# Kernel tuning notes

Measured on AMD Instinct MI355X. Metric: run time of the kernel, lower is better.

## Reference

```python
import jax, jax.numpy as jnp
import numpy as np

N, E, B = 8000, 128000, 16
DIN, D, H, C, L = 16, 256, 8, 32, 6
MC, NT = 200, 8
NEG_SLOPE = 0.2


def layernorm(x, s, b):
    mu = jnp.mean(x, axis=-1, keepdims=True)
    var = jnp.mean(jnp.square(x - mu), axis=-1, keepdims=True)
    return (x - mu) * jax.lax.rsqrt(var + 1e-5) * s + b


def setup_inputs() -> dict:
    key = jax.random.key(0)
    ks = iter(jax.random.split(key, 64))
    rn = lambda shape, s=0.05: jax.random.normal(next(ks), shape, jnp.float32) * s
    inp = {}
    inp['x'] = jax.random.normal(next(ks), (N, DIN), jnp.float32)
    inp['edge_index'] = jax.random.randint(next(ks), (2, E), 0, N)
    inp['batch'] = jnp.sort(jax.random.randint(next(ks), (N,), 0, B))
    # node encoder: Linear(DIN,D) + LayerNorm
    inp['enc_W'] = rn((DIN, D)); inp['enc_b'] = jnp.zeros((D,), jnp.float32)
    inp['enc_ls'] = jnp.ones((D,), jnp.float32); inp['enc_lb'] = jnp.zeros((D,), jnp.float32)
    # GATv2 layers (stacked): lin_l, lin_r, att, output bias, post LayerNorm
    inp['Wl'] = rn((L, D, D)); inp['bl'] = jnp.zeros((L, D), jnp.float32)
    inp['Wr'] = rn((L, D, D)); inp['br'] = jnp.zeros((L, D), jnp.float32)
    inp['att'] = rn((L, H, C))
    inp['gb'] = jnp.zeros((L, D), jnp.float32)
    inp['gls'] = jnp.ones((L, D), jnp.float32); inp['glb'] = jnp.zeros((L, D), jnp.float32)
    # color head MLP: D -> D -> D//2 -> MC
    inp['cW1'] = rn((D, D)); inp['cb1'] = jnp.zeros((D,), jnp.float32)
    inp['cW2'] = rn((D, D // 2)); inp['cb2'] = jnp.zeros((D // 2,), jnp.float32)
    inp['cW3'] = rn((D // 2, MC)); inp['cb3'] = jnp.zeros((MC,), jnp.float32)
    # chromatic head: 2D -> D -> D//2 -> MC
    inp['chW1'] = rn((2 * D, D)); inp['chb1'] = jnp.zeros((D,), jnp.float32)
    inp['chW2'] = rn((D, D // 2)); inp['chb2'] = jnp.zeros((D // 2,), jnp.float32)
    inp['chW3'] = rn((D // 2, MC)); inp['chb3'] = jnp.zeros((MC,), jnp.float32)
    # type head: 2D -> 128 -> NT
    inp['tW1'] = rn((2 * D, 128)); inp['tb1'] = jnp.zeros((128,), jnp.float32)
    inp['tW2'] = rn((128, NT)); inp['tb2'] = jnp.zeros((NT,), jnp.float32)
    # difficulty head: 2D -> 64 -> 1, sigmoid * 100
    inp['dW1'] = rn((2 * D, 64)); inp['db1'] = jnp.zeros((64,), jnp.float32)
    inp['dW2'] = rn((64, 1)); inp['db2'] = jnp.zeros((1,), jnp.float32)
    return inp


def reference(x, edge_index, batch, enc_W, enc_b, enc_ls, enc_lb,
              Wl, bl, Wr, br, att, gb, gls, glb,
              cW1, cb1, cW2, cb2, cW3, cb3,
              chW1, chb1, chW2, chb2, chW3, chb3,
              tW1, tb1, tW2, tb2, dW1, db1, dW2, db2):
    n = x.shape[0]
    # node encoder (dropout = identity at inference)
    h = jax.nn.relu(layernorm(x @ enc_W + enc_b, enc_ls, enc_lb))
    # add self loops once (same for every layer)
    sl = jnp.arange(n)
    src = jnp.concatenate([edge_index[0], sl])  # message source j
    dst = jnp.concatenate([edge_index[1], sl])  # message target i
    for i in range(L):
        xl = (h @ Wl[i] + bl[i]).reshape(n, H, C)  # source transform
        xr = (h @ Wr[i] + br[i]).reshape(n, H, C)  # target transform
        # GATv2 attention: a^T LeakyReLU(xl_j + xr_i)
        e = jax.nn.leaky_relu(xl[src] + xr[dst], NEG_SLOPE)  # [E+N, H, C]
        logits = jnp.einsum('ehc,hc->eh', e, att[i])          # [E+N, H]
        # segment softmax over destination node (self-loops guarantee denom > 0)
        m = jax.ops.segment_max(logits, dst, num_segments=n)
        m = jnp.where(jnp.isfinite(m), m, 0.0)
        p = jnp.exp(logits - m[dst])
        denom = jax.ops.segment_sum(p, dst, num_segments=n)
        alpha = p / denom[dst]
        out = jax.ops.segment_sum(xl[src] * alpha[:, :, None], dst, num_segments=n)
        out = out.reshape(n, D) + gb[i]
        h_new = jax.nn.elu(layernorm(out, gls[i], glb[i]))
        h = h + h_new if i > 0 else h_new
    # per-node color logits
    z = jax.nn.relu(h @ cW1 + cb1)
    z = jax.nn.relu(z @ cW2 + cb2)
    node_colors = z @ cW3 + cb3
    # global mean/max pooling per graph
    cnt = jax.ops.segment_sum(jnp.ones((n,), h.dtype), batch, num_segments=B)
    mean_p = jax.ops.segment_sum(h, batch, num_segments=B) / jnp.maximum(cnt, 1.0)[:, None]
    max_p = jax.ops.segment_max(h, batch, num_segments=B)
    max_p = jnp.where(jnp.isfinite(max_p), max_p, 0.0)
    g = jnp.concatenate([mean_p, max_p], axis=1)  # [B, 2D]
    zc = jax.nn.relu(g @ chW1 + chb1)
    zc = jax.nn.relu(zc @ chW2 + chb2)
    chromatic_num = zc @ chW3 + chb3
    zt = jax.nn.relu(g @ tW1 + tb1)
    graph_type = zt @ tW2 + tb2
    zd = jax.nn.relu(g @ dW1 + db1)
    difficulty = jax.nn.sigmoid(zd @ dW2 + db2) * 100.0
    return (node_colors, chromatic_num, graph_type, difficulty)
```

## Files before the change

### kernel.cpp

```cpp
#include <hip/hip_runtime.h>
#include <hip/hip_bf16.h>

constexpr int DIN = 16;
constexpr int D   = 256;
constexpr int NH  = 8;
constexpr int NC  = 32;
constexpr int MC  = 200;
constexpr int NT  = 8;
constexpr int BG  = 16;
constexpr int NL  = 6;
constexpr int PS  = 16;
constexpr float NEG = 0.2f;

typedef __attribute__((ext_vector_type(8))) short bfrag;
typedef __attribute__((ext_vector_type(4))) float f32x4;

__device__ inline unsigned short f2bf(float f) {
    unsigned int u = __float_as_uint(f);
    u += 0x7FFFu + ((u >> 16) & 1u);
    return (unsigned short)(u >> 16);
}
__device__ inline float bf2f(unsigned short u) {
    return __uint_as_float((unsigned int)u << 16);
}

__device__ inline float dot_ilp(const float* g, const float* __restrict__ W, int K, int ldw, int t) {
    float a0 = 0.f, a1 = 0.f, a2 = 0.f, a3 = 0.f;
    for (int k = 0; k < K; k += 4) {
        a0 = fmaf(g[k + 0], W[(k + 0) * ldw + t], a0);
        a1 = fmaf(g[k + 1], W[(k + 1) * ldw + t], a1);
        a2 = fmaf(g[k + 2], W[(k + 2) * ldw + t], a2);
        a3 = fmaf(g[k + 3], W[(k + 3) * ldw + t], a3);
    }
    return (a0 + a1) + (a2 + a3);
}


__device__ inline void enc_node(const float* x, const float* W, const float* b, const float* ls,
                                const float* lb, float* h, int n, int lane) {
    int c4 = lane * 4;
    float xs[DIN];
#pragma unroll
    for (int k = 0; k < DIN; k += 4) {
        float4 xv = *(const float4*)&x[n * DIN + k];
        xs[k] = xv.x; xs[k + 1] = xv.y; xs[k + 2] = xv.z; xs[k + 3] = xv.w;
    }
    float4 a = *(const float4*)&b[c4];
#pragma unroll
    for (int k = 0; k < DIN; k++) {
        float4 wv = *(const float4*)&W[k * D + c4];
        a.x = fmaf(xs[k], wv.x, a.x);
        a.y = fmaf(xs[k], wv.y, a.y);
        a.z = fmaf(xs[k], wv.z, a.z);
        a.w = fmaf(xs[k], wv.w, a.w);
    }
    float s = a.x + a.y + a.z + a.w;
#pragma unroll
    for (int msk = 1; msk <= 32; msk <<= 1) s += __shfl_xor(s, msk);
    float mu = s * (1.f / D);
    float4 dv = make_float4(a.x - mu, a.y - mu, a.z - mu, a.w - mu);
    float v2 = dv.x * dv.x + dv.y * dv.y + dv.z * dv.z + dv.w * dv.w;
#pragma unroll
    for (int msk = 1; msk <= 32; msk <<= 1) v2 += __shfl_xor(v2, msk);
    float rstd = rsqrtf(v2 * (1.f / D) + 1e-5f);
    float4 lsv = *(const float4*)&ls[c4];
    float4 lbv = *(const float4*)&lb[c4];
    float4 y = make_float4(fmaxf(dv.x * rstd * lsv.x + lbv.x, 0.f),
                           fmaxf(dv.y * rstd * lsv.y + lbv.y, 0.f),
                           fmaxf(dv.z * rstd * lsv.z + lbv.z, 0.f),
                           fmaxf(dv.w * rstd * lsv.w + lbv.w, 0.f));
    *(float4*)&h[(size_t)n * D + c4] = y;
}

__device__ inline float4 attn_compute(const unsigned short* xl, const unsigned short* xr,
                                      const int* row_ptr, const int* col, const float* att,
                                      const float* gb, const float* gls, const float* glb,
                                      const float* h, int layer, int n, int lane) {
    int c4 = lane * 4;
    ushort4 xr4 = *(const ushort4*)&xr[(size_t)n * D + c4];
    float4 xrv = make_float4(bf2f(xr4.x), bf2f(xr4.y), bf2f(xr4.z), bf2f(xr4.w));
    float4 av  = *(const float4*)&att[c4];
    int beg = row_ptr[n], end = row_ptr[n + 1];
    int deg = end - beg;
    int myc = col[beg + min(lane, deg - 1)];
    float l = 0.f;
    float4 acc = make_float4(0.f, 0.f, 0.f, 0.f);
    auto loadx = [&](int i) -> ushort4 {
        if (i < deg) {
            int s = (i < 64) ? __shfl(myc, i) : col[beg + i];
            return *(const ushort4*)&xl[(size_t)s * D + c4];
        }
        return make_ushort4(0, 0, 0, 0);
    };
    auto step = [&](ushort4 x4) {
        float4 xlv = make_float4(bf2f(x4.x), bf2f(x4.y), bf2f(x4.z), bf2f(x4.w));
        float sx = xlv.x + xrv.x; sx = sx > 0.f ? sx : NEG * sx;
        float sy = xlv.y + xrv.y; sy = sy > 0.f ? sy : NEG * sy;
        float sz = xlv.z + xrv.z; sz = sz > 0.f ? sz : NEG * sz;
        float sw = xlv.w + xrv.w; sw = sw > 0.f ? sw : NEG * sw;
        float z = av.x * sx + av.y * sy + av.z * sz + av.w * sw;
        z += __shfl_xor(z, 1); z += __shfl_xor(z, 2); z += __shfl_xor(z, 4);
        float p = __expf(z);
        l += p;
        acc.x = fmaf(p, xlv.x, acc.x);
        acc.y = fmaf(p, xlv.y, acc.y);
        acc.z = fmaf(p, xlv.z, acc.z);
        acc.w = fmaf(p, xlv.w, acc.w);
    };
    ushort4 b0 = loadx(0), b1 = loadx(1), b2 = loadx(2), b3 = loadx(3);
    int e = 0;
    for (; e + 4 <= deg; e += 4) {
        ushort4 n0 = loadx(e + 4), n1 = loadx(e + 5), n2 = loadx(e + 6), n3 = loadx(e + 7);
        step(b0); step(b1); step(b2); step(b3);
        b0 = n0; b1 = n1; b2 = n2; b3 = n3;
    }
    if (e + 0 < deg) step(b0);
    if (e + 1 < deg) step(b1);
    if (e + 2 < deg) step(b2);
    float4 gbv = *(const float4*)&gb[c4];
    float rl = 1.f / l;
    float4 o = make_float4(acc.x * rl + gbv.x, acc.y * rl + gbv.y,
                           acc.z * rl + gbv.z, acc.w * rl + gbv.w);
    float s = o.x + o.y + o.z + o.w;
#pragma unroll
    for (int msk = 1; msk <= 32; msk <<= 1) s += __shfl_xor(s, msk);
    float mu = s * (1.f / D);
    float4 dv = make_float4(o.x - mu, o.y - mu, o.z - mu, o.w - mu);
    float v2 = dv.x * dv.x + dv.y * dv.y + dv.z * dv.z + dv.w * dv.w;
#pragma unroll
    for (int msk = 1; msk <= 32; msk <<= 1) v2 += __shfl_xor(v2, msk);
    float rstd = rsqrtf(v2 * (1.f / D) + 1e-5f);
    float4 glsv = *(const float4*)&gls[c4];
    float4 glbv = *(const float4*)&glb[c4];
    float y0 = dv.x * rstd * glsv.x + glbv.x;
    float y1 = dv.y * rstd * glsv.y + glbv.y;
    float y2 = dv.z * rstd * glsv.z + glbv.z;
    float y3 = dv.w * rstd * glsv.w + glbv.w;
    y0 = y0 > 0.f ? y0 : expm1f(y0);
    y1 = y1 > 0.f ? y1 : expm1f(y1);
    y2 = y2 > 0.f ? y2 : expm1f(y2);
    y3 = y3 > 0.f ? y3 : expm1f(y3);
    float4 prev = make_float4(0.f, 0.f, 0.f, 0.f);
    if (layer > 0) prev = *(const float4*)&h[(size_t)n * D + c4];
    return make_float4(prev.x + y0, prev.y + y1, prev.z + y2, prev.w + y3);
}

__device__ inline void attn2(const unsigned short* xl, const unsigned short* xr,
                             const int* row_ptr, const int* col, const float* att,
                             const float* gb, const float* gls, const float* glb,
                             const float* h, int layer, int n0, int n1, int N, int lane,
                             float4& out0, float4& out1) {
    int c4 = lane * 4;
    float4 av = *(const float4*)&att[c4];
    bool v1 = (n1 < N);
    ushort4 x40 = *(const ushort4*)&xr[(size_t)n0 * D + c4];
    float4 xrv0 = make_float4(bf2f(x40.x), bf2f(x40.y), bf2f(x40.z), bf2f(x40.w));
    float4 xrv1 = make_float4(0.f, 0.f, 0.f, 0.f);
    if (v1) {
        ushort4 x41 = *(const ushort4*)&xr[(size_t)n1 * D + c4];
        xrv1 = make_float4(bf2f(x41.x), bf2f(x41.y), bf2f(x41.z), bf2f(x41.w));
    }
    int beg0 = row_ptr[n0], deg0 = row_ptr[n0 + 1] - beg0;
    int beg1 = v1 ? row_ptr[n1] : 0;
    int deg1 = v1 ? (row_ptr[n1 + 1] - beg1) : 0;
    int myc0 = col[beg0 + min(lane, deg0 - 1)];
    int myc1 = v1 ? col[beg1 + min(lane, deg1 - 1)] : 0;
    float l0 = 0.f, l1 = 0.f;
    float4 a0 = make_float4(0.f, 0.f, 0.f, 0.f);
    float4 a1 = make_float4(0.f, 0.f, 0.f, 0.f);
    auto load0 = [&](int i) -> ushort4 {
        if (i < deg0) {
            int s = (i < 64) ? __shfl(myc0, i) : col[beg0 + i];
            return *(const ushort4*)&xl[(size_t)s * D + c4];
        }
        return make_ushort4(0, 0, 0, 0);
    };
    auto load1 = [&](int i) -> ushort4 {
        if (i < deg1) {
            int s = (i < 64) ? __shfl(myc1, i) : col[beg1 + i];
            return *(const ushort4*)&xl[(size_t)s * D + c4];
        }
        return make_ushort4(0, 0, 0, 0);
    };
    auto step0 = [&](ushort4 x4) {
        float4 xlv = make_float4(bf2f(x4.x), bf2f(x4.y), bf2f(x4.z), bf2f(x4.w));
        float sx = xlv.x + xrv0.x; sx = sx > 0.f ? sx : NEG * sx;
        float sy = xlv.y + xrv0.y; sy = sy > 0.f ? sy : NEG * sy;
        float sz = xlv.z + xrv0.z; sz = sz > 0.f ? sz : NEG * sz;
        float sw = xlv.w + xrv0.w; sw = sw > 0.f ? sw : NEG * sw;
        float z = av.x * sx + av.y * sy + av.z * sz + av.w * sw;
        z += __shfl_xor(z, 1); z += __shfl_xor(z, 2); z += __shfl_xor(z, 4);
        float p = __expf(z);
        l0 += p;
        a0.x = fmaf(p, xlv.x, a0.x);
        a0.y = fmaf(p, xlv.y, a0.y);
        a0.z = fmaf(p, xlv.z, a0.z);
        a0.w = fmaf(p, xlv.w, a0.w);
    };
    auto step1 = [&](ushort4 x4) {
        float4 xlv = make_float4(bf2f(x4.x), bf2f(x4.y), bf2f(x4.z), bf2f(x4.w));
        float sx = xlv.x + xrv1.x; sx = sx > 0.f ? sx : NEG * sx;
        float sy = xlv.y + xrv1.y; sy = sy > 0.f ? sy : NEG * sy;
        float sz = xlv.z + xrv1.z; sz = sz > 0.f ? sz : NEG * sz;
        float sw = xlv.w + xrv1.w; sw = sw > 0.f ? sw : NEG * sw;
        float z = av.x * sx + av.y * sy + av.z * sz + av.w * sw;
        z += __shfl_xor(z, 1); z += __shfl_xor(z, 2); z += __shfl_xor(z, 4);
        float p = __expf(z);
        l1 += p;
        a1.x = fmaf(p, xlv.x, a1.x);
        a1.y = fmaf(p, xlv.y, a1.y);
        a1.z = fmaf(p, xlv.z, a1.z);
        a1.w = fmaf(p, xlv.w, a1.w);
    };
    ushort4 p00 = load0(0), p01 = load0(1), p02 = load0(2), p03 = load0(3);
    ushort4 p10 = load1(0), p11 = load1(1), p12 = load1(2), p13 = load1(3);
    int mx = max(deg0, deg1);
    for (int e = 0; e < mx; e += 4) {
        ushort4 q00 = load0(e + 4), q01 = load0(e + 5), q02 = load0(e + 6), q03 = load0(e + 7);
        ushort4 q10 = load1(e + 4), q11 = load1(e + 5), q12 = load1(e + 6), q13 = load1(e + 7);
        if (e < deg0)     step0(p00);
        if (e < deg1)     step1(p10);
        if (e + 1 < deg0) step0(p01);
        if (e + 1 < deg1) step1(p11);
        if (e + 2 < deg0) step0(p02);
        if (e + 2 < deg1) step1(p12);
        if (e + 3 < deg0) step0(p03);
        if (e + 3 < deg1) step1(p13);
        p00 = q00; p01 = q01; p02 = q02; p03 = q03;
        p10 = q10; p11 = q11; p12 = q12; p13 = q13;
    }
    float4 gbv = *(const float4*)&gb[c4];
    float4 glsv = *(const float4*)&gls[c4];
    float4 glbv = *(const float4*)&glb[c4];
    auto epilogue = [&](float4 acc, float l, int n) -> float4 {
        float rl = 1.f / l;
        float4 o = make_float4(acc.x * rl + gbv.x, acc.y * rl + gbv.y,
                               acc.z * rl + gbv.z, acc.w * rl + gbv.w);
        float s = o.x + o.y + o.z + o.w;
#pragma unroll
        for (int msk = 1; msk <= 32; msk <<= 1) s += __shfl_xor(s, msk);
        float mu = s * (1.f / D);
        float4 dv = make_float4(o.x - mu, o.y - mu, o.z - mu, o.w - mu);
        float v2 = dv.x * dv.x + dv.y * dv.y + dv.z * dv.z + dv.w * dv.w;
#pragma unroll
        for (int msk = 1; msk <= 32; msk <<= 1) v2 += __shfl_xor(v2, msk);
        float rstd = rsqrtf(v2 * (1.f / D) + 1e-5f);
        float y0 = dv.x * rstd * glsv.x + glbv.x;
        float y1 = dv.y * rstd * glsv.y + glbv.y;
        float y2 = dv.z * rstd * glsv.z + glbv.z;
        float y3 = dv.w * rstd * glsv.w + glbv.w;
        y0 = y0 > 0.f ? y0 : expm1f(y0);
        y1 = y1 > 0.f ? y1 : expm1f(y1);
        y2 = y2 > 0.f ? y2 : expm1f(y2);
        y3 = y3 > 0.f ? y3 : expm1f(y3);
        float4 prev = make_float4(0.f, 0.f, 0.f, 0.f);
        if (layer > 0) prev = *(const float4*)&h[(size_t)n * D + c4];
        return make_float4(prev.x + y0, prev.y + y1, prev.z + y2, prev.w + y3);
    };
    out0 = epilogue(a0, l0, n0);
    if (v1) out1 = epilogue(a1, l1, n1);
    else    out1 = make_float4(0.f, 0.f, 0.f, 0.f);
}

__device__ inline void gemm_one_ct(const unsigned short (*As)[264],
                                   const unsigned short* WpL, const unsigned short* WpR,
                                   const float* bl, const float* br,
                                   unsigned short* xl, unsigned short* xr,
                                   int N, int nb, int ctg, int lane) {
    int m = lane & 15, q = lane >> 4;
    float bLv = bl[ctg * 16 + m];
    float bRv = br[ctg * 16 + m];
    f32x4 accL = (f32x4){bLv, bLv, bLv, bLv};
    f32x4 accR = (f32x4){bRv, bRv, bRv, bRv};
#pragma unroll
    for (int ks = 0; ks < 8; ks++) {
        bfrag af = *(const bfrag*)&As[m][ks * 32 + q * 8];
        size_t off = (((size_t)ctg * 8 + ks) * 64 + lane) * 8;
        bfrag bL = *(const bfrag*)&WpL[off];
        bfrag bR = *(const bfrag*)&WpR[off];
        accL = __builtin_amdgcn_mfma_f32_16x16x32_bf16(af, bL, accL, 0, 0, 0);
        accR = __builtin_amdgcn_mfma_f32_16x16x32_bf16(af, bR, accR, 0, 0, 0);
    }
    int colg = ctg * 16 + m;
#pragma unroll
    for (int reg = 0; reg < 4; reg++) {
        int row = nb + q * 4 + reg;
        if (row < N) {
            xl[(size_t)row * D + colg] = f2bf(accL[reg]);
            xr[(size_t)row * D + colg] = f2bf(accR[reg]);
        }
    }
}

__device__ inline void gemm_core(const unsigned short (*As)[264],
                                 const unsigned short* WpL, const unsigned short* WpR,
                                 const float* bl, const float* br,
                                 unsigned short* xl, unsigned short* xr, int N, int nb, int T) {
    int lane = T & 63, w = T >> 6;
#pragma unroll
    for (int ct = 0; ct < 4; ct++)
        gemm_one_ct(As, WpL, WpR, bl, br, xl, xr, N, nb, w * 4 + ct, lane);
}

__device__ inline void repack_attn_one(const float* Wl, const float* Wr, unsigned short* Wp, int tid) {
    int lane = tid & 63;
    int r1 = tid >> 6;
    int ks = r1 & 7;
    int r2 = r1 >> 3;
    int ct = r2 & 15;
    int mi = r2 >> 4;
    int layer = mi >> 1, mat = mi & 1;
    const float* W = (mat == 0 ? Wl : Wr) + (size_t)layer * D * D;
    int n = ct * 16 + (lane & 15);
    int kb = ks * 32 + (lane >> 4) * 8;
    size_t base = (((size_t)(mi * 16 + ct) * 8 + ks) * 64 + lane) * 8;
#pragma unroll
    for (int j = 0; j < 8; j++) Wp[base + j] = f2bf(W[(size_t)(kb + j) * D + n]);
}

__device__ inline void repack_gen_one(const float* W, unsigned short* Wp, int K, int NCOL, int nks, int tid) {
    int lane = tid & 63;
    int r = tid >> 6;
    int ks = r % nks;
    int ct = r / nks;
    int n = ct * 16 + (lane & 15);
    int kb = ks * 32 + (lane >> 4) * 8;
    size_t base = (((size_t)ct * nks + ks) * 64 + lane) * 8;
#pragma unroll
    for (int j = 0; j < 8; j++) {
        int k = kb + j;
        Wp[base + j] = (n < NCOL && k < K) ? f2bf(W[(size_t)k * NCOL + n]) : (unsigned short)0;
    }
}


__global__ __launch_bounds__(256) void init_enc_k(const float* __restrict__ x, const float* __restrict__ W,
                                                  const float* __restrict__ b, const float* __restrict__ ls,
                                                  const float* __restrict__ lb, float* __restrict__ h,
                                                  int* __restrict__ deg, int N) {
    int gid = blockIdx.x * 256 + threadIdx.x;
    if (gid < N) deg[gid] = 1;
    int lane = threadIdx.x & 63;
    int n = blockIdx.x * 4 + (threadIdx.x >> 6);
    if (n < N) enc_node(x, W, b, ls, lb, h, n, lane);
}

__global__ __launch_bounds__(256) void count_repack_k(const int* __restrict__ dst, int* __restrict__ deg, int E,
                                                      const float* __restrict__ Wl, const float* __restrict__ Wr,
                                                      unsigned short* __restrict__ Wp,
                                                      const float* __restrict__ cW1, unsigned short* __restrict__ cW1p,
                                                      const float* __restrict__ cW2, unsigned short* __restrict__ cW2p,
                                                      const float* __restrict__ cW3, unsigned short* __restrict__ cW3p) {
    int gid = blockIdx.x * 256 + threadIdx.x;
    if (gid < E) atomicAdd(&deg[dst[gid]], 1);
    if (gid < NL * 2 * 16 * 8 * 64) repack_attn_one(Wl, Wr, Wp, gid);
    if (gid < 16 * 8 * 64) repack_gen_one(cW1, cW1p, D, D, 8, gid);
    if (gid < 8 * 8 * 64)  repack_gen_one(cW2, cW2p, D, 128, 8, gid);
    if (gid < 13 * 4 * 64) repack_gen_one(cW3, cW3p, 128, MC, 4, gid);
}

__global__ __launch_bounds__(1024) void scan_k(const int* __restrict__ deg, int* __restrict__ row_ptr,
                                               int* __restrict__ fill, int N) {
    __shared__ int sd[1024];
    int t = threadIdx.x;
    int chunk = (N + 1023) >> 10;
    int lo = t * chunk, hi = min(lo + chunk, N);
    int s = 0;
    for (int i = lo; i < hi; i++) s += deg[i];
    sd[t] = s;
    __syncthreads();
    for (int off = 1; off < 1024; off <<= 1) {
        int v = (t >= off) ? sd[t - off] : 0;
        __syncthreads();
        sd[t] += v;
        __syncthreads();
    }
    int run = (t > 0) ? sd[t - 1] : 0;
    for (int i = lo; i < hi; i++) {
        row_ptr[i] = run; fill[i] = run;
        run += deg[i];
    }
    if (t == 1023) row_ptr[N] = sd[1023];
}

__global__ __launch_bounds__(256) void scatter_gemm0_k(const int* __restrict__ src, const int* __restrict__ dst,
                                                       int* __restrict__ fill, int* __restrict__ col, int E, int N,
                                                       const float* __restrict__ h,
                                                       const unsigned short* __restrict__ WpL,
                                                       const unsigned short* __restrict__ WpR,
                                                       const float* __restrict__ bl, const float* __restrict__ br,
                                                       unsigned short* __restrict__ xl, unsigned short* __restrict__ xr) {
    __shared__ unsigned short As[16][264];
    int T = threadIdx.x;
    int tt = blockIdx.x;
    int ntiles = (N + 15) >> 4;
    if (tt < ntiles) {
        int nb = tt * 16;
#pragma unroll
        for (int r = 0; r < 16; r++) {
            int row = nb + r;
            float v = (row < N) ? h[(size_t)row * D + T] : 0.f;
            As[r][T] = f2bf(v);
        }
        __syncthreads();
        gemm_core(As, WpL, WpR, bl, br, xl, xr, N, nb, T);
    }
    for (int e = blockIdx.x * 256 + T; e < E + N; e += gridDim.x * 256) {
        if (e < E) {
            int p = atomicAdd(&fill[dst[e]], 1);
            col[p] = src[e];
        } else {
            int n = e - E;
            int p = atomicAdd(&fill[n], 1);
            col[p] = n;
        }
    }
}

__global__ __launch_bounds__(1024, 4) void layer_k(const unsigned short* __restrict__ xl_in,
                                                   const unsigned short* __restrict__ xr_in,
                                                   const int* __restrict__ row_ptr, const int* __restrict__ col,
                                                   const float* __restrict__ att, const float* __restrict__ gb,
                                                   const float* __restrict__ gls, const float* __restrict__ glb,
                                                   float* __restrict__ h, int layer, int N,
                                                   const unsigned short* __restrict__ WpL,
                                                   const unsigned short* __restrict__ WpR,
                                                   const float* __restrict__ bl, const float* __restrict__ br,
                                                   unsigned short* __restrict__ xl_out, unsigned short* __restrict__ xr_out) {
    __shared__ unsigned short As[32][264];
    int T = threadIdx.x;
    int lane = T & 63, wv = T >> 6;
    int nb = blockIdx.x * 32;
    int c4 = lane * 4;
    int n0 = nb + wv, n1 = nb + wv + 16;
    if (n0 < N) {
        float4 r0, r1;
        attn2(xl_in, xr_in, row_ptr, col, att, gb, gls, glb, h, layer, n0, n1, N, lane, r0, r1);
        *(float4*)&h[(size_t)n0 * D + c4] = r0;
        As[wv][c4 + 0] = f2bf(r0.x);
        As[wv][c4 + 1] = f2bf(r0.y);
        As[wv][c4 + 2] = f2bf(r0.z);
        As[wv][c4 + 3] = f2bf(r0.w);
        if (n1 < N) {
            *(float4*)&h[(size_t)n1 * D + c4] = r1;
            As[wv + 16][c4 + 0] = f2bf(r1.x);
            As[wv + 16][c4 + 1] = f2bf(r1.y);
            As[wv + 16][c4 + 2] = f2bf(r1.z);
            As[wv + 16][c4 + 3] = f2bf(r1.w);
        } else {
            As[wv + 16][c4 + 0] = 0; As[wv + 16][c4 + 1] = 0;
            As[wv + 16][c4 + 2] = 0; As[wv + 16][c4 + 3] = 0;
        }
    } else {
        As[wv][c4 + 0] = 0; As[wv][c4 + 1] = 0; As[wv][c4 + 2] = 0; As[wv][c4 + 3] = 0;
        As[wv + 16][c4 + 0] = 0; As[wv + 16][c4 + 1] = 0;
        As[wv + 16][c4 + 2] = 0; As[wv + 16][c4 + 3] = 0;
    }
    __syncthreads();
    gemm_one_ct((const unsigned short (*)[264])&As[0],  WpL, WpR, bl, br, xl_out, xr_out, N, nb,      wv, lane);
    gemm_one_ct((const unsigned short (*)[264])&As[16], WpL, WpR, bl, br, xl_out, xr_out, N, nb + 16, wv, lane);
}

__global__ __launch_bounds__(1024) void last_k(const unsigned short* __restrict__ xl_in,
                                               const unsigned short* __restrict__ xr_in,
                                               const int* __restrict__ row_ptr, const int* __restrict__ col,
                                               const float* __restrict__ att, const float* __restrict__ gb,
                                               const float* __restrict__ gls, const float* __restrict__ glb,
                                               float* __restrict__ h, int N,
                                               const unsigned short* __restrict__ W1p, const float* __restrict__ b1,
                                               const unsigned short* __restrict__ W2p, const float* __restrict__ b2,
                                               const unsigned short* __restrict__ W3p, const float* __restrict__ b3,
                                               float* __restrict__ out) {
    __shared__ unsigned short As[16][264];
    __shared__ unsigned short Zs[16][264];
    int T = threadIdx.x;
    int lane = T & 63, wv = T >> 6;
    int nb = blockIdx.x * 16;
    int c4 = lane * 4;
    int n = nb + wv;
    if (n < N) {
        float4 res = attn_compute(xl_in, xr_in, row_ptr, col, att, gb, gls, glb, h, NL - 1, n, lane);
        *(float4*)&h[(size_t)n * D + c4] = res;
        As[wv][c4 + 0] = f2bf(res.x);
        As[wv][c4 + 1] = f2bf(res.y);
        As[wv][c4 + 2] = f2bf(res.z);
        As[wv][c4 + 3] = f2bf(res.w);
    } else {
        As[wv][c4 + 0] = 0; As[wv][c4 + 1] = 0; As[wv][c4 + 2] = 0; As[wv][c4 + 3] = 0;
    }
    __syncthreads();
    int m = lane & 15, q = lane >> 4;
    {
        float bv = b1[wv * 16 + m];
        f32x4 acc = (f32x4){bv, bv, bv, bv};
#pragma unroll
        for (int ks = 0; ks < 8; ks++) {
            bfrag af = *(const bfrag*)&As[m][ks * 32 + q * 8];
            bfrag bf = *(const bfrag*)&W1p[(((size_t)wv * 8 + ks) * 64 + lane) * 8];
            acc = __builtin_amdgcn_mfma_f32_16x16x32_bf16(af, bf, acc, 0, 0, 0);
        }
        int colg = wv * 16 + m;
#pragma unroll
        for (int reg = 0; reg < 4; reg++)
            Zs[q * 4 + reg][colg] = f2bf(fmaxf(acc[reg], 0.f));
    }
    __syncthreads();
    if (wv < 8) {
        float bv = b2[wv * 16 + m];
        f32x4 acc = (f32x4){bv, bv, bv, bv};
#pragma unroll
        for (int ks = 0; ks < 8; ks++) {
            bfrag af = *(const bfrag*)&Zs[m][ks * 32 + q * 8];
            bfrag bf = *(const bfrag*)&W2p[(((size_t)wv * 8 + ks) * 64 + lane) * 8];
            acc = __builtin_amdgcn_mfma_f32_16x16x32_bf16(af, bf, acc, 0, 0, 0);
        }
        int colg = wv * 16 + m;
#pragma unroll
        for (int reg = 0; reg < 4; reg++)
            As[q * 4 + reg][colg] = f2bf(fmaxf(acc[reg], 0.f));
    }
    __syncthreads();
    if (wv < 13) {
        int colg = wv * 16 + m;
        float bv = (colg < MC) ? b3[colg] : 0.f;
        f32x4 acc = (f32x4){bv, bv, bv, bv};
#pragma unroll
        for (int ks = 0; ks < 4; ks++) {
            bfrag af = *(const bfrag*)&As[m][ks * 32 + q * 8];
            bfrag bf = *(const bfrag*)&W3p[(((size_t)wv * 4 + ks) * 64 + lane) * 8];
            acc = __builtin_amdgcn_mfma_f32_16x16x32_bf16(af, bf, acc, 0, 0, 0);
        }
#pragma unroll
        for (int reg = 0; reg < 4; reg++) {
            int row = nb + q * 4 + reg;
            if (row < N && colg < MC) out[(size_t)row * MC + colg] = acc[reg];
        }
    }
}

__global__ __launch_bounds__(256) void pool_k(const float* __restrict__ h, const int* __restrict__ batch,
                                              float* __restrict__ psum, float* __restrict__ pmax,
                                              int* __restrict__ cnt, int N) {
    int b = blockIdx.x;
    int sl = blockIdx.y;
    int c = threadIdx.x;
    int lo = 0, hi = N;
    while (lo < hi) { int mid = (lo + hi) >> 1; if (batch[mid] < b) lo = mid + 1; else hi = mid; }
    int s0 = lo;
    lo = 0; hi = N;
    while (lo < hi) { int mid = (lo + hi) >> 1; if (batch[mid] < b + 1) lo = mid + 1; else hi = mid; }
    int s1 = lo;
    int len = s1 - s0;
    int chunk = (len + PS - 1) / PS;
    int n0 = s0 + sl * chunk;
    int n1 = min(n0 + chunk, s1);
    float sum = 0.f, mx = -3.0e38f;
    for (int n = n0; n < n1; n++) {
        float v = h[(size_t)n * D + c];
        sum += v;
        mx = fmaxf(mx, v);
    }
    psum[(size_t)(b * PS + sl) * D + c] = sum;
    pmax[(size_t)(b * PS + sl) * D + c] = mx;
    if (c == 0 && sl == 0) cnt[b] = len;
}

__global__ __launch_bounds__(256) void heads_k(const float* __restrict__ psum, const float* __restrict__ pmax,
                                               const int* __restrict__ cnt,
                                               const float* __restrict__ chW1, const float* __restrict__ chb1,
                                               const float* __restrict__ chW2, const float* __restrict__ chb2,
                                               const float* __restrict__ chW3, const float* __restrict__ chb3,
                                               const float* __restrict__ tW1, const float* __restrict__ tb1,
                                               const float* __restrict__ tW2, const float* __restrict__ tb2,
                                               const float* __restrict__ dW1, const float* __restrict__ db1,
                                               const float* __restrict__ dW2, const float* __restrict__ db2,
                                               float* __restrict__ out_ch, float* __restrict__ out_t,
                                               float* __restrict__ out_d) {
    int b = blockIdx.x, sec = blockIdx.y, t = threadIdx.x;
    __shared__ float g[2 * D];
    __shared__ float z1[D];
    __shared__ float z2[128];
    float sum = 0.f, mx = -3.0e38f;
#pragma unroll
    for (int sl = 0; sl < PS; sl++) {
        sum += psum[(size_t)(b * PS + sl) * D + t];
        mx = fmaxf(mx, pmax[(size_t)(b * PS + sl) * D + t]);
    }
    int cn = cnt[b];
    float c = fmaxf((float)cn, 1.f);
    g[t] = sum / c;
    g[D + t] = (cn > 0) ? mx : 0.f;
    __syncthreads();
    if (sec == 0) {
        z1[t] = fmaxf(chb1[t] + dot_ilp(g, chW1, 2 * D, D, t), 0.f);
        __syncthreads();
        if (t < 128) z2[t] = fmaxf(chb2[t] + dot_ilp(z1, chW2, D, 128, t), 0.f);
        __syncthreads();
        if (t < MC) out_ch[b * MC + t] = chb3[t] + dot_ilp(z2, chW3, 128, MC, t);
    } else if (sec == 1) {
        if (t < 128) z1[t] = fmaxf(tb1[t] + dot_ilp(g, tW1, 2 * D, 128, t), 0.f);
        __syncthreads();
        if (t < NT) out_t[b * NT + t] = tb2[t] + dot_ilp(z1, tW2, 128, NT, t);
    } else {
        if (t < 64) z1[t] = fmaxf(db1[t] + dot_ilp(g, dW1, 2 * D, 64, t), 0.f);
        __syncthreads();
        if (t == 0) {
            float a = db2[0] + dot_ilp(z1, dW2, 64, 1, 0);
            out_d[b] = 100.f / (1.f + __expf(-a));
        }
    }
}

extern "C" void kernel_launch(void* const* d_in, const int* in_sizes, int n_in,
                              void* d_out, int out_size, void* d_ws, size_t ws_size,
                              hipStream_t stream) {
    const float* x     = (const float*)d_in[0];
    const int*   ei    = (const int*)d_in[1];
    const int*   batch = (const int*)d_in[2];
    const float* encW  = (const float*)d_in[3];
    const float* encb  = (const float*)d_in[4];
    const float* encls = (const float*)d_in[5];
    const float* enclb = (const float*)d_in[6];
    const float* Wl    = (const float*)d_in[7];
    const float* bl    = (const float*)d_in[8];
    const float* Wr    = (const float*)d_in[9];
    const float* br    = (const float*)d_in[10];
    const float* att   = (const float*)d_in[11];
    const float* gb    = (const float*)d_in[12];
    const float* gls   = (const float*)d_in[13];
    const float* glb   = (const float*)d_in[14];
    const float* cW1   = (const float*)d_in[15];
    const float* cb1   = (const float*)d_in[16];
    const float* cW2   = (const float*)d_in[17];
    const float* cb2   = (const float*)d_in[18];
    const float* cW3   = (const float*)d_in[19];
    const float* cb3   = (const float*)d_in[20];
    const float* chW1  = (const float*)d_in[21];
    const float* chb1  = (const float*)d_in[22];
    const float* chW2  = (const float*)d_in[23];
    const float* chb2  = (const float*)d_in[24];
    const float* chW3  = (const float*)d_in[25];
    const float* chb3  = (const float*)d_in[26];
    const float* tW1   = (const float*)d_in[27];
    const float* tb1   = (const float*)d_in[28];
    const float* tW2   = (const float*)d_in[29];
    const float* tb2   = (const float*)d_in[30];
    const float* dW1   = (const float*)d_in[31];
    const float* db1   = (const float*)d_in[32];
    const float* dW2   = (const float*)d_in[33];
    const float* db2   = (const float*)d_in[34];

    const int N = in_sizes[0] / DIN;
    const int E = in_sizes[1] / 2;
    const int* esrc = ei;
    const int* edst = ei + E;

    char* p = (char*)d_ws;
    auto carve = [&](size_t bytes) { char* r = p; p += (bytes + 255) & ~(size_t)255; return r; };
    int*            row_ptr = (int*)carve((size_t)(N + 1) * 4);
    int*            fill    = (int*)carve((size_t)N * 4);
    int*            deg     = (int*)carve((size_t)N * 4);
    int*            cnt     = (int*)carve((size_t)BG * 4);
    float*          psum    = (float*)carve((size_t)BG * PS * D * 4);
    float*          pmax    = (float*)carve((size_t)BG * PS * D * 4);
    int*            col     = (int*)carve((size_t)(E + N) * 4);
    unsigned short* Wp      = (unsigned short*)carve((size_t)NL * 2 * 65536 * 2);
    unsigned short* cW1p    = (unsigned short*)carve((size_t)16 * 8 * 64 * 8 * 2);
    unsigned short* cW2p    = (unsigned short*)carve((size_t)8 * 8 * 64 * 8 * 2);
    unsigned short* cW3p    = (unsigned short*)carve((size_t)13 * 4 * 64 * 8 * 2);
    float*          h       = (float*)carve((size_t)N * D * 4);
    unsigned short* xlA     = (unsigned short*)carve((size_t)N * D * 2);
    unsigned short* xrA     = (unsigned short*)carve((size_t)N * D * 2);
    unsigned short* xlB     = (unsigned short*)carve((size_t)N * D * 2);
    unsigned short* xrB     = (unsigned short*)carve((size_t)N * D * 2);
    (void)ws_size; (void)n_in; (void)out_size;

    const int ntiles16 = (N + 15) / 16;
    const int ntiles32 = (N + 31) / 32;
    const int sblocks = max(ntiles16, (E + N + 255) / 256);

    init_enc_k<<<(N + 3) / 4, 256, 0, stream>>>(x, encW, encb, encls, enclb, h, deg, N);
    count_repack_k<<<512, 256, 0, stream>>>(edst, deg, E, Wl, Wr, Wp, cW1, cW1p, cW2, cW2p, cW3, cW3p);
    scan_k<<<1, 1024, 0, stream>>>(deg, row_ptr, fill, N);
    scatter_gemm0_k<<<sblocks, 256, 0, stream>>>(esrc, edst, fill, col, E, N, h,
                                                 Wp + 0, Wp + (size_t)65536,
                                                 bl + 0, br + 0, xlA, xrA);
    for (int l = 0; l < NL - 1; l++) {
        const unsigned short* xin_l = (l & 1) ? xlB : xlA;
        const unsigned short* xin_r = (l & 1) ? xrB : xrA;
        unsigned short* xout_l = (l & 1) ? xlA : xlB;
        unsigned short* xout_r = (l & 1) ? xrA : xrB;
        layer_k<<<ntiles32, 1024, 0, stream>>>(xin_l, xin_r, row_ptr, col, att + l * NH * NC,
                                               gb + l * D, gls + l * D, glb + l * D, h, l, N,
                                               Wp + (size_t)((l + 1) * 2 + 0) * 65536,
                                               Wp + (size_t)((l + 1) * 2 + 1) * 65536,
                                               bl + (l + 1) * D, br + (l + 1) * D, xout_l, xout_r);
    }
    float* out = (float*)d_out;
    last_k<<<ntiles16, 1024, 0, stream>>>(xlB, xrB, row_ptr, col, att + (NL - 1) * NH * NC,
                                          gb + (NL - 1) * D, gls + (NL - 1) * D, glb + (NL - 1) * D, h, N,
                                          cW1p, cb1, cW2p, cb2, cW3p, cb3, out);
    pool_k<<<dim3(BG, PS), 256, 0, stream>>>(h, batch, psum, pmax, cnt, N);
    heads_k<<<dim3(BG, 3), 256, 0, stream>>>(psum, pmax, cnt, chW1, chb1, chW2, chb2, chW3, chb3,
                                             tW1, tb1, tW2, tb2, dW1, db1, dW2, db2,
                                             out + (size_t)N * MC,
                                             out + (size_t)N * MC + BG * MC,
                                             out + (size_t)N * MC + BG * MC + BG * NT);
}
```

Measured before the change: 423.9 us.

## Split fused attention+GEMM layer kernel into separate attention and projection kernels

Replaces the fused per-layer kernel (attention aggregation for 32 nodes followed by in-block bf16 MFMA projection) with two kernels: a small-block attention kernel, one wave per node, writing h in fp32, and a separate GEMM kernel that reloads h and computes the next layer's xl/xr. The final layer's attention and color head are split the same way. This is meant to raise occupancy and remove the load imbalance where the whole 1024-thread block waits on its slowest node before the GEMM. In exchange it adds kernel launches and an extra round trip of h through global memory per layer.

```diff
diff --git a/kernel.cpp b/kernel.cpp
--- a/kernel.cpp
+++ b/kernel.cpp
@@ -145,123 +145,6 @@
     return make_float4(prev.x + y0, prev.y + y1, prev.z + y2, prev.w + y3);
 }
 
-__device__ inline void attn2(const unsigned short* xl, const unsigned short* xr,
-                             const int* row_ptr, const int* col, const float* att,
-                             const float* gb, const float* gls, const float* glb,
-                             const float* h, int layer, int n0, int n1, int N, int lane,
-                             float4& out0, float4& out1) {
-    int c4 = lane * 4;
-    float4 av = *(const float4*)&att[c4];
-    bool v1 = (n1 < N);
-    ushort4 x40 = *(const ushort4*)&xr[(size_t)n0 * D + c4];
-    float4 xrv0 = make_float4(bf2f(x40.x), bf2f(x40.y), bf2f(x40.z), bf2f(x40.w));
-    float4 xrv1 = make_float4(0.f, 0.f, 0.f, 0.f);
-    if (v1) {
-        ushort4 x41 = *(const ushort4*)&xr[(size_t)n1 * D + c4];
-        xrv1 = make_float4(bf2f(x41.x), bf2f(x41.y), bf2f(x41.z), bf2f(x41.w));
-    }
-    int beg0 = row_ptr[n0], deg0 = row_ptr[n0 + 1] - beg0;
-    int beg1 = v1 ? row_ptr[n1] : 0;
-    int deg1 = v1 ? (row_ptr[n1 + 1] - beg1) : 0;
-    int myc0 = col[beg0 + min(lane, deg0 - 1)];
-    int myc1 = v1 ? col[beg1 + min(lane, deg1 - 1)] : 0;
-    float l0 = 0.f, l1 = 0.f;
-    float4 a0 = make_float4(0.f, 0.f, 0.f, 0.f);
-    float4 a1 = make_float4(0.f, 0.f, 0.f, 0.f);
-    auto load0 = [&](int i) -> ushort4 {
-        if (i < deg0) {
-            int s = (i < 64) ? __shfl(myc0, i) : col[beg0 + i];
-            return *(const ushort4*)&xl[(size_t)s * D + c4];
-        }
-        return make_ushort4(0, 0, 0, 0);
-    };
-    auto load1 = [&](int i) -> ushort4 {
-        if (i < deg1) {
-            int s = (i < 64) ? __shfl(myc1, i) : col[beg1 + i];
-            return *(const ushort4*)&xl[(size_t)s * D + c4];
-        }
-        return make_ushort4(0, 0, 0, 0);
-    };
-    auto step0 = [&](ushort4 x4) {
-        float4 xlv = make_float4(bf2f(x4.x), bf2f(x4.y), bf2f(x4.z), bf2f(x4.w));
-        float sx = xlv.x + xrv0.x; sx = sx > 0.f ? sx : NEG * sx;
-        float sy = xlv.y + xrv0.y; sy = sy > 0.f ? sy : NEG * sy;
-        float sz = xlv.z + xrv0.z; sz = sz > 0.f ? sz : NEG * sz;
-        float sw = xlv.w + xrv0.w; sw = sw > 0.f ? sw : NEG * sw;
-        float z = av.x * sx + av.y * sy + av.z * sz + av.w * sw;
-        z += __shfl_xor(z, 1); z += __shfl_xor(z, 2); z += __shfl_xor(z, 4);
-        float p = __expf(z);
-        l0 += p;
-        a0.x = fmaf(p, xlv.x, a0.x);
-        a0.y = fmaf(p, xlv.y, a0.y);
-        a0.z = fmaf(p, xlv.z, a0.z);
-        a0.w = fmaf(p, xlv.w, a0.w);
-    };
-    auto step1 = [&](ushort4 x4) {
-        float4 xlv = make_float4(bf2f(x4.x), bf2f(x4.y), bf2f(x4.z), bf2f(x4.w));
-        float sx = xlv.x + xrv1.x; sx = sx > 0.f ? sx : NEG * sx;
-        float sy = xlv.y + xrv1.y; sy = sy > 0.f ? sy : NEG * sy;
-        float sz = xlv.z + xrv1.z; sz = sz > 0.f ? sz : NEG * sz;
-        float sw = xlv.w + xrv1.w; sw = sw > 0.f ? sw : NEG * sw;
-        float z = av.x * sx + av.y * sy + av.z * sz + av.w * sw;
-        z += __shfl_xor(z, 1); z += __shfl_xor(z, 2); z += __shfl_xor(z, 4);
-        float p = __expf(z);
-        l1 += p;
-        a1.x = fmaf(p, xlv.x, a1.x);
-        a1.y = fmaf(p, xlv.y, a1.y);
-        a1.z = fmaf(p, xlv.z, a1.z);
-        a1.w = fmaf(p, xlv.w, a1.w);
-    };
-    ushort4 p00 = load0(0), p01 = load0(1), p02 = load0(2), p03 = load0(3);
-    ushort4 p10 = load1(0), p11 = load1(1), p12 = load1(2), p13 = load1(3);
-    int mx = max(deg0, deg1);
-    for (int e = 0; e < mx; e += 4) {
-        ushort4 q00 = load0(e + 4), q01 = load0(e + 5), q02 = load0(e + 6), q03 = load0(e + 7);
-        ushort4 q10 = load1(e + 4), q11 = load1(e + 5), q12 = load1(e + 6), q13 = load1(e + 7);
-        if (e < deg0)     step0(p00);
-        if (e < deg1)     step1(p10);
-        if (e + 1 < deg0) step0(p01);
-        if (e + 1 < deg1) step1(p11);
-        if (e + 2 < deg0) step0(p02);
-        if (e + 2 < deg1) step1(p12);
-        if (e + 3 < deg0) step0(p03);
-        if (e + 3 < deg1) step1(p13);
-        p00 = q00; p01 = q01; p02 = q02; p03 = q03;
-        p10 = q10; p11 = q11; p12 = q12; p13 = q13;
-    }
-    float4 gbv = *(const float4*)&gb[c4];
-    float4 glsv = *(const float4*)&gls[c4];
-    float4 glbv = *(const float4*)&glb[c4];
-    auto epilogue = [&](float4 acc, float l, int n) -> float4 {
-        float rl = 1.f / l;
-        float4 o = make_float4(acc.x * rl + gbv.x, acc.y * rl + gbv.y,
-                               acc.z * rl + gbv.z, acc.w * rl + gbv.w);
-        float s = o.x + o.y + o.z + o.w;
-#pragma unroll
-        for (int msk = 1; msk <= 32; msk <<= 1) s += __shfl_xor(s, msk);
-        float mu = s * (1.f / D);
-        float4 dv = make_float4(o.x - mu, o.y - mu, o.z - mu, o.w - mu);
-        float v2 = dv.x * dv.x + dv.y * dv.y + dv.z * dv.z + dv.w * dv.w;
-#pragma unroll
-        for (int msk = 1; msk <= 32; msk <<= 1) v2 += __shfl_xor(v2, msk);
-        float rstd = rsqrtf(v2 * (1.f / D) + 1e-5f);
-        float y0 = dv.x * rstd * glsv.x + glbv.x;
-        float y1 = dv.y * rstd * glsv.y + glbv.y;
-        float y2 = dv.z * rstd * glsv.z + glbv.z;
-        float y3 = dv.w * rstd * glsv.w + glbv.w;
-        y0 = y0 > 0.f ? y0 : expm1f(y0);
-        y1 = y1 > 0.f ? y1 : expm1f(y1);
-        y2 = y2 > 0.f ? y2 : expm1f(y2);
-        y3 = y3 > 0.f ? y3 : expm1f(y3);
-        float4 prev = make_float4(0.f, 0.f, 0.f, 0.f);
-        if (layer > 0) prev = *(const float4*)&h[(size_t)n * D + c4];
-        return make_float4(prev.x + y0, prev.y + y1, prev.z + y2, prev.w + y3);
-    };
-    out0 = epilogue(a0, l0, n0);
-    if (v1) out1 = epilogue(a1, l1, n1);
-    else    out1 = make_float4(0.f, 0.f, 0.f, 0.f);
-}
-
 __device__ inline void gemm_one_ct(const unsigned short (*As)[264],
                                    const unsigned short* WpL, const unsigned short* WpR,
                                    const float* bl, const float* br,
@@ -417,60 +300,44 @@
     }
 }
 
-__global__ __launch_bounds__(1024, 4) void layer_k(const unsigned short* __restrict__ xl_in,
-                                                   const unsigned short* __restrict__ xr_in,
-                                                   const int* __restrict__ row_ptr, const int* __restrict__ col,
-                                                   const float* __restrict__ att, const float* __restrict__ gb,
-                                                   const float* __restrict__ gls, const float* __restrict__ glb,
-                                                   float* __restrict__ h, int layer, int N,
-                                                   const unsigned short* __restrict__ WpL,
-                                                   const unsigned short* __restrict__ WpR,
-                                                   const float* __restrict__ bl, const float* __restrict__ br,
-                                                   unsigned short* __restrict__ xl_out, unsigned short* __restrict__ xr_out) {
-    __shared__ unsigned short As[32][264];
+__global__ __launch_bounds__(256, 8) void attn_k(const unsigned short* __restrict__ xl_in,
+                                                 const unsigned short* __restrict__ xr_in,
+                                                 const int* __restrict__ row_ptr, const int* __restrict__ col,
+                                                 const float* __restrict__ att, const float* __restrict__ gb,
+                                                 const float* __restrict__ gls, const float* __restrict__ glb,
+                                                 float* __restrict__ h, int layer, int N) {
     int T = threadIdx.x;
     int lane = T & 63, wv = T >> 6;
-    int nb = blockIdx.x * 32;
-    int c4 = lane * 4;
-    int n0 = nb + wv, n1 = nb + wv + 16;
-    if (n0 < N) {
-        float4 r0, r1;
-        attn2(xl_in, xr_in, row_ptr, col, att, gb, gls, glb, h, layer, n0, n1, N, lane, r0, r1);
-        *(float4*)&h[(size_t)n0 * D + c4] = r0;
-        As[wv][c4 + 0] = f2bf(r0.x);
-        As[wv][c4 + 1] = f2bf(r0.y);
-        As[wv][c4 + 2] = f2bf(r0.z);
-        As[wv][c4 + 3] = f2bf(r0.w);
-        if (n1 < N) {
-            *(float4*)&h[(size_t)n1 * D + c4] = r1;
-            As[wv + 16][c4 + 0] = f2bf(r1.x);
-            As[wv + 16][c4 + 1] = f2bf(r1.y);
-            As[wv + 16][c4 + 2] = f2bf(r1.z);
-            As[wv + 16][c4 + 3] = f2bf(r1.w);
-        } else {
-            As[wv + 16][c4 + 0] = 0; As[wv + 16][c4 + 1] = 0;
-            As[wv + 16][c4 + 2] = 0; As[wv + 16][c4 + 3] = 0;
-        }
-    } else {
-        As[wv][c4 + 0] = 0; As[wv][c4 + 1] = 0; As[wv][c4 + 2] = 0; As[wv][c4 + 3] = 0;
-        As[wv + 16][c4 + 0] = 0; As[wv + 16][c4 + 1] = 0;
-        As[wv + 16][c4 + 2] = 0; As[wv + 16][c4 + 3] = 0;
+    int n = blockIdx.x * 4 + wv;
+    if (n >= N) return;
+    float4 res = attn_compute(xl_in, xr_in, row_ptr, col, att, gb, gls, glb, h, layer, n, lane);
+    *(float4*)&h[(size_t)n * D + lane * 4] = res;
+}
+
+__global__ __launch_bounds__(256, 4) void gemm_lr_k(const float* __restrict__ h,
+                                                    const unsigned short* __restrict__ WpL,
+                                                    const unsigned short* __restrict__ WpR,
+                                                    const float* __restrict__ bl, const float* __restrict__ br,
+                                                    unsigned short* __restrict__ xl, unsigned short* __restrict__ xr,
+                                                    int N) {
+    __shared__ unsigned short As[16][264];
+    int T = threadIdx.x;
+    int nb = blockIdx.x * 16;
+#pragma unroll
+    for (int r = 0; r < 16; r++) {
+        int row = nb + r;
+        float v = (row < N) ? h[(size_t)row * D + T] : 0.f;
+        As[r][T] = f2bf(v);
     }
     __syncthreads();
-    gemm_one_ct((const unsigned short (*)[264])&As[0],  WpL, WpR, bl, br, xl_out, xr_out, N, nb,      wv, lane);
-    gemm_one_ct((const unsigned short (*)[264])&As[16], WpL, WpR, bl, br, xl_out, xr_out, N, nb + 16, wv, lane);
-}
-
-__global__ __launch_bounds__(1024) void last_k(const unsigned short* __restrict__ xl_in,
-                                               const unsigned short* __restrict__ xr_in,
-                                               const int* __restrict__ row_ptr, const int* __restrict__ col,
-                                               const float* __restrict__ att, const float* __restrict__ gb,
-                                               const float* __restrict__ gls, const float* __restrict__ glb,
-                                               float* __restrict__ h, int N,
-                                               const unsigned short* __restrict__ W1p, const float* __restrict__ b1,
-                                               const unsigned short* __restrict__ W2p, const float* __restrict__ b2,
-                                               const unsigned short* __restrict__ W3p, const float* __restrict__ b3,
-                                               float* __restrict__ out) {
+    gemm_core(As, WpL, WpR, bl, br, xl, xr, N, nb, T);
+}
+
+__global__ __launch_bounds__(1024) void colorhead_k(const float* __restrict__ h, int N,
+                                                    const unsigned short* __restrict__ W1p, const float* __restrict__ b1,
+                                                    const unsigned short* __restrict__ W2p, const float* __restrict__ b2,
+                                                    const unsigned short* __restrict__ W3p, const float* __restrict__ b3,
+                                                    float* __restrict__ out) {
     __shared__ unsigned short As[16][264];
     __shared__ unsigned short Zs[16][264];
     int T = threadIdx.x;
@@ -479,12 +346,11 @@
     int c4 = lane * 4;
     int n = nb + wv;
     if (n < N) {
-        float4 res = attn_compute(xl_in, xr_in, row_ptr, col, att, gb, gls, glb, h, NL - 1, n, lane);
-        *(float4*)&h[(size_t)n * D + c4] = res;
-        As[wv][c4 + 0] = f2bf(res.x);
-        As[wv][c4 + 1] = f2bf(res.y);
-        As[wv][c4 + 2] = f2bf(res.z);
-        As[wv][c4 + 3] = f2bf(res.w);
+        float4 v = *(const float4*)&h[(size_t)n * D + c4];
+        As[wv][c4 + 0] = f2bf(v.x);
+        As[wv][c4 + 1] = f2bf(v.y);
+        As[wv][c4 + 2] = f2bf(v.z);
+        As[wv][c4 + 3] = f2bf(v.w);
     } else {
         As[wv][c4 + 0] = 0; As[wv][c4 + 1] = 0; As[wv][c4 + 2] = 0; As[wv][c4 + 3] = 0;
     }
@@ -676,7 +542,7 @@
     (void)ws_size; (void)n_in; (void)out_size;
 
     const int ntiles16 = (N + 15) / 16;
-    const int ntiles32 = (N + 31) / 32;
+    const int nblk4    = (N + 3) / 4;
     const int sblocks = max(ntiles16, (E + N + 255) / 256);
 
     init_enc_k<<<(N + 3) / 4, 256, 0, stream>>>(x, encW, encb, encls, enclb, h, deg, N);
@@ -690,16 +556,18 @@
         const unsigned short* xin_r = (l & 1) ? xrB : xrA;
         unsigned short* xout_l = (l & 1) ? xlA : xlB;
         unsigned short* xout_r = (l & 1) ? xrA : xrB;
-        layer_k<<<ntiles32, 1024, 0, stream>>>(xin_l, xin_r, row_ptr, col, att + l * NH * NC,
-                                               gb + l * D, gls + l * D, glb + l * D, h, l, N,
-                                               Wp + (size_t)((l + 1) * 2 + 0) * 65536,
-                                               Wp + (size_t)((l + 1) * 2 + 1) * 65536,
-                                               bl + (l + 1) * D, br + (l + 1) * D, xout_l, xout_r);
+        attn_k<<<nblk4, 256, 0, stream>>>(xin_l, xin_r, row_ptr, col, att + l * NH * NC,
+                                          gb + l * D, gls + l * D, glb + l * D, h, l, N);
+        gemm_lr_k<<<ntiles16, 256, 0, stream>>>(h,
+                                                Wp + (size_t)((l + 1) * 2 + 0) * 65536,
+                                                Wp + (size_t)((l + 1) * 2 + 1) * 65536,
+                                                bl + (l + 1) * D, br + (l + 1) * D, xout_l, xout_r, N);
     }
     float* out = (float*)d_out;
-    last_k<<<ntiles16, 1024, 0, stream>>>(xlB, xrB, row_ptr, col, att + (NL - 1) * NH * NC,
-                                          gb + (NL - 1) * D, gls + (NL - 1) * D, glb + (NL - 1) * D, h, N,
-                                          cW1p, cb1, cW2p, cb2, cW3p, cb3, out);
+    attn_k<<<nblk4, 256, 0, stream>>>(xlB, xrB, row_ptr, col, att + (NL - 1) * NH * NC,
+                                      gb + (NL - 1) * D, gls + (NL - 1) * D, glb + (NL - 1) * D,
+                                      h, NL - 1, N);
+    colorhead_k<<<ntiles16, 1024, 0, stream>>>(h, N, cW1p, cb1, cW2p, cb2, cW3p, cb3, out);
     pool_k<<<dim3(BG, PS), 256, 0, stream>>>(h, batch, psum, pmax, cnt, N);
     heads_k<<<dim3(BG, 3), 256, 0, stream>>>(psum, pmax, cnt, chW1, chb1, chW2, chb2, chW3, chb3,
                                              tW1, tb1, tW2, tb2, dW1, db1, dW2, db2,
```

Result: no change. 419.8 us (-1.0%).
